# Kernel optimization log

Hardware: AMD Instinct MI355X
Metric: run time of the kernel (lower is better)

The kernel has to match this reference:

```python
import jax, jax.numpy as jnp
import numpy as np

B, C, H, W = 16, 256, 64, 64
K = 1024


def setup_inputs() -> dict:
    key = jax.random.key(0)
    k1, k2 = jax.random.split(key)
    z = jax.random.normal(k1, (B, C, H, W), dtype=jnp.float32)
    codebook = jax.random.normal(k2, (K, C), dtype=jnp.float32)
    return {"z": z, "codebook": codebook}


def reference(z, codebook):
    # assign: nearest-code indices via squared euclidean distance
    b, c, h, w = z.shape
    zf = jnp.transpose(z, (0, 2, 3, 1)).reshape(-1, c)            # [N, C]
    # ||z||^2 - 2 z.cb^T + ||cb||^2  -> [N, K]
    dists = (jnp.sum(zf * zf, axis=1, keepdims=True)
             - 2.0 * jnp.einsum('nc,kc->nk', zf, codebook)
             + jnp.sum(codebook * codebook, axis=1)[None, :])
    idx = jnp.argmin(dists, axis=1)                                # [N]
    indices = idx.reshape(b, 1, h, w)                              # [B,1,H,W]
    # embed_code: gather codebook rows, back to BCHW
    zq = codebook[idx].reshape(b, h, w, c)                         # [B,H,W,C]
    zq = jnp.transpose(zq, (0, 3, 1, 2))                           # [B,C,H,W]
    return zq, indices
```

## Files before the change

### kernel.cpp

```cpp
#include <hip/hip_runtime.h>


#define HWSZ 4096
#define CDIM 256
#define KCODES 1024
#define NPIX 65536
#define ZQ_ELEMS (16 * 256 * 4096)
#define MARGIN 0.75f

#define WS_CBSWZ 0
#define WS_CBN64 524288
#define WS_CBN32 532480
#define WS_CNT   536576
#define WS_LISTS 536592

typedef __attribute__((ext_vector_type(8))) short bf16x8;
typedef __attribute__((ext_vector_type(4))) float f32x4;
typedef __attribute__((ext_vector_type(4))) unsigned short us4;

#define MFMA16(a, b, c) __builtin_amdgcn_mfma_f32_16x16x32_bf16(a, b, c, 0, 0, 0)

__device__ __forceinline__ unsigned short f2bf(float f) {
  unsigned u = __float_as_uint(f);
  unsigned r = u + 0x7FFFu + ((u >> 16) & 1u);
  return (unsigned short)(r >> 16);
}

__device__ __forceinline__ void gload_lds16(const void* g, void* l) {
  __builtin_amdgcn_global_load_lds(
      (const __attribute__((address_space(1))) unsigned int*)g,
      (__attribute__((address_space(3))) unsigned int*)l, 16, 0, 0);
}

__device__ __forceinline__ void ins3(unsigned& k1, unsigned& k2, unsigned& k3,
                                     unsigned k) {
  unsigned nk2, nk3;
  asm("v_med3_u32 %0, %1, %2, %3" : "=v"(nk2) : "v"(k1), "v"(k2), "v"(k));
  asm("v_med3_u32 %0, %1, %2, %3" : "=v"(nk3) : "v"(k2), "v"(k3), "v"(k));
  k1 = k1 < k ? k1 : k;
  k2 = nk2;
  k3 = nk3;
}

__device__ __forceinline__ float keyf(unsigned k) {
  return __uint_as_float(k & 0xFFFFFC00u);
}

__global__ void vq_prep(const float* __restrict__ cb,
                        unsigned short* __restrict__ cbswz,
                        double* __restrict__ cbn64,
                        float* __restrict__ cbn32p,
                        int* __restrict__ cnt) {
  const int t = threadIdx.x;
  if (blockIdx.x == 0 && t == 0) { cnt[0] = 0; cnt[1] = 0; }
  const int code = blockIdx.x * 4 + (t >> 6);
  const int lane = t & 63;
  const int c4 = lane * 4;

  float4 v = *(const float4*)(cb + (size_t)code * CDIM + c4);
  us4 hv;
  hv.x = f2bf(-2.f * v.x); hv.y = f2bf(-2.f * v.y);
  hv.z = f2bf(-2.f * v.z); hv.w = f2bf(-2.f * v.w);
  const int K = (code >> 9) * 32 + ((code >> 4) & 31);
  const int kk = c4 >> 5;
  const int lg = (c4 >> 3) & 3;
  const int within = (c4 & 7) * 2;
  size_t off = (size_t)K * 8192 + kk * 1024 + (code & 15) * 64 + lg * 16 + within;
  *(us4*)((char*)cbswz + off) = hv;

  double s = (double)v.x * v.x;
  s = fma((double)v.y, (double)v.y, s);
  s = fma((double)v.z, (double)v.z, s);
  s = fma((double)v.w, (double)v.w, s);
#pragma unroll
  for (int o = 32; o; o >>= 1) s += __shfl_xor(s, o, 64);
  if (lane == 0) {
    cbn64[code] = s;
    cbn32p[code] = (float)s + 512.0f;
  }
}

__launch_bounds__(256)
__global__ void vq_stage1(const float* __restrict__ z,
                          const float* __restrict__ cb,
                          const unsigned short* __restrict__ cbswz,
                          const float* __restrict__ cbn32p,
                          float* __restrict__ out_zq,
                          float* __restrict__ out_idx,
                          int* __restrict__ cnt,
                          int* __restrict__ listA, int capA,
                          int* __restrict__ listB, int capB,
                          float* __restrict__ zws, int zcap) {
  extern __shared__ char smem[];
  const int t = threadIdx.x;
  const int w = t >> 6;
  const int lane = t & 63;
  const int lg = lane >> 4;
  const int lcode = lane & 15;
  const int h = w >> 1;
  const int q = w & 1;
  const int p0 = blockIdx.x * 64;
  const int b = p0 >> 12;
  const int hw0 = p0 & (HWSZ - 1);
  const float* zb = z + (size_t)b * (CDIM * HWSZ) + hw0;

  char* const bb0 = smem + q * 8192;
  char* const bb1 = smem + 16384 + q * 8192;
  char* const bb2 = smem + 32768 + q * 8192;
  float* nrm = (float*)(smem + 49152);
  char* scratch = smem + 49152;

  const int stl = h * 4096 + lane * 16;
  const char* cbbase = (const char*)cbswz + (size_t)q * 262144 + stl;

#define STAGE(CIDX, SBUF)                                             \
  {                                                                   \
    const char* gs_ = cbbase + ((size_t)(CIDX) << 13);                \
    char* ld_ = (SBUF) + stl;                                         \
    gload_lds16(gs_, ld_);                                            \
    gload_lds16(gs_ + 1024, ld_ + 1024);                              \
    gload_lds16(gs_ + 2048, ld_ + 2048);                              \
    gload_lds16(gs_ + 3072, ld_ + 3072);                              \
  }

  STAGE(0, bb0);
  STAGE(1, bb1);

  bf16x8 af[2][8];
#pragma unroll
  for (int T = 0; T < 2; ++T) {
    const float* zr = zb + (h * 32 + T * 16 + lcode);
#pragma unroll
    for (int kk = 0; kk < 8; ++kk) {
      const int ch0 = kk * 32 + lg * 8;
      bf16x8 f;
#pragma unroll
      for (int j = 0; j < 8; ++j)
        f[j] = (short)f2bf(zr[(size_t)(ch0 + j) * HWSZ]);
      af[T][kk] = f;
    }
  }

  *(float4*)(nrm + t * 4) = *(const float4*)(cbn32p + t * 4);
  __syncthreads();

  unsigned k1[2][4], k2[2][4], k3[2][4];
#pragma unroll
  for (int T = 0; T < 2; ++T)
#pragma unroll
    for (int q4 = 0; q4 < 4; ++q4) {
      k1[T][q4] = 0xFFFFFFFFu; k2[T][q4] = 0xFFFFFFFFu; k3[T][q4] = 0xFFFFFFFFu;
    }

  const int bq = lcode * 64 + lg * 16;
  const float* nrmp = nrm + q * 512 + lcode;
  const int kbase = q * 512 + lcode;

#define BODY(CIDX, RBUF, SBUF, DOSTAGE, WN)                           \
  {                                                                   \
    asm volatile("s_waitcnt vmcnt(" WN ")" ::: "memory");             \
    __builtin_amdgcn_s_barrier();                                     \
    __builtin_amdgcn_sched_barrier(0);                                \
    if (DOSTAGE) STAGE((CIDX) + 2, SBUF);                             \
    const char* pb_ = (RBUF) + bq;                                    \
    f32x4 acc0 = {0.f, 0.f, 0.f, 0.f};                                \
    f32x4 acc1 = {0.f, 0.f, 0.f, 0.f};                                \
    _Pragma("unroll")                                                 \
    for (int kk = 0; kk < 8; ++kk) {                                  \
      bf16x8 bf_ = *(const bf16x8*)(pb_ + kk * 1024);                 \
      acc0 = MFMA16(af[0][kk], bf_, acc0);                            \
      acc1 = MFMA16(af[1][kk], bf_, acc1);                            \
    }                                                                 \
    const unsigned code_ = (unsigned)(kbase + (CIDX) * 16);           \
    const float cn_ = nrmp[(CIDX) * 16];                              \
    _Pragma("unroll")                                                 \
    for (int q4 = 0; q4 < 4; ++q4) {                                  \
      float m0_ = cn_ + acc0[q4];                                     \
      ins3(k1[0][q4], k2[0][q4], k3[0][q4],                           \
           (__float_as_uint(m0_) & 0xFFFFFC00u) | code_);             \
      float m1_ = cn_ + acc1[q4];                                     \
      ins3(k1[1][q4], k2[1][q4], k3[1][q4],                           \
           (__float_as_uint(m1_) & 0xFFFFFC00u) | code_);             \
    }                                                                 \
  }

#pragma unroll 1
  for (int c3 = 0; c3 < 30; c3 += 3) {
    BODY(c3 + 0, bb0, bb2, 1, "4");
    BODY(c3 + 1, bb1, bb0, 1, "4");
    BODY(c3 + 2, bb2, bb1, 1, "4");
  }
  BODY(30, bb0, bb2, 0, "4");
  BODY(31, bb1, bb0, 0, "0");
#undef BODY
#undef STAGE

#pragma unroll
  for (int mask = 1; mask <= 8; mask <<= 1) {
#pragma unroll
    for (int T = 0; T < 2; ++T)
#pragma unroll
      for (int q4 = 0; q4 < 4; ++q4) {
        unsigned o1 = __shfl_xor(k1[T][q4], mask, 64);
        unsigned o2 = __shfl_xor(k2[T][q4], mask, 64);
        unsigned o3 = __shfl_xor(k3[T][q4], mask, 64);
        ins3(k1[T][q4], k2[T][q4], k3[T][q4], o1);
        ins3(k1[T][q4], k2[T][q4], k3[T][q4], o2);
        ins3(k1[T][q4], k2[T][q4], k3[T][q4], o3);
      }
  }

  unsigned* mk = (unsigned*)scratch;
  int* sbest = (int*)(scratch + 1536);
  int* flp = (int*)(scratch + 1792);
  int* flq = (int*)(scratch + 2048);
  int* lcnt = (int*)(scratch + 2304);
  if (t == 0) *lcnt = 0;
  if (lcode == 0) {
#pragma unroll
    for (int T = 0; T < 2; ++T)
#pragma unroll
      for (int q4 = 0; q4 < 4; ++q4) {
        int row = h * 32 + T * 16 + lg * 4 + q4;
        unsigned* d = mk + (row * 2 + q) * 3;
        d[0] = k1[T][q4]; d[1] = k2[T][q4]; d[2] = k3[T][q4];
      }
  }
  __syncthreads();

  if (t < 64) {
    unsigned a1 = mk[t * 6 + 0], a2 = mk[t * 6 + 1], a3 = mk[t * 6 + 2];
    ins3(a1, a2, a3, mk[t * 6 + 3]);
    ins3(a1, a2, a3, mk[t * 6 + 4]);
    ins3(a1, a2, a3, mk[t * 6 + 5]);
    const int p = p0 + t;
    const int i1 = (int)(a1 & 1023u);
    sbest[t] = i1;
    out_idx[p] = (float)i1;
    float f1 = keyf(a1);
    float g2 = keyf(a2) - f1;
    float g3 = keyf(a3) - f1;
    if (g3 < MARGIN) {
      int pos = atomicAdd(cnt + 1, 1);
      if (pos < capB) listB[pos] = p;
    } else if (g2 < MARGIN) {
      int pos = atomicAdd(cnt, 1);
      if (pos < capA) {
        listA[2 * pos] = p | (i1 << 16);
        listA[2 * pos + 1] = (int)(a2 & 1023u) | ((int)(a3 & 1023u) << 16);
        if (pos < zcap) {
          int li = atomicAdd(lcnt, 1);
          flp[li] = p;
          flq[li] = pos;
        }
      }
    }
  }
  __syncthreads();

  {
    const int px = t & 63;
    const int best = sbest[px];
    const int ch0g = (t >> 6) * 64;
    const float* crow = cb + (size_t)best * CDIM + ch0g;
    float* ob = out_zq + (size_t)b * (CDIM * HWSZ) + (size_t)ch0g * HWSZ + hw0 + px;
#pragma unroll 4
    for (int c2 = 0; c2 < 64; c2 += 4) {
      float4 v = *(const float4*)(crow + c2);
      ob[(size_t)(c2 + 0) * HWSZ] = v.x;
      ob[(size_t)(c2 + 1) * HWSZ] = v.y;
      ob[(size_t)(c2 + 2) * HWSZ] = v.z;
      ob[(size_t)(c2 + 3) * HWSZ] = v.w;
    }
  }

  {
    const int nf = *lcnt;
    for (int e = 0; e < nf; ++e) {
      const int p = flp[e];
      const int slot = flq[e];
      const int bb = p >> 12;
      const int hh = p & (HWSZ - 1);
      zws[(size_t)slot * 256 + t] =
          z[(size_t)bb * (CDIM * HWSZ) + (size_t)t * HWSZ + hh];
    }
  }
}

__launch_bounds__(256)
__global__ void vq_resolve3(const float* __restrict__ z,
                            const float* __restrict__ cb,
                            const double* __restrict__ cbn64,
                            float* __restrict__ out_zq,
                            float* __restrict__ out_idx,
                            const int* __restrict__ cnt,
                            const int* __restrict__ listA, int capA,
                            const float* __restrict__ zws, int zcap) {
  const int lane = threadIdx.x & 63;
  const int wid = (blockIdx.x * blockDim.x + threadIdx.x) >> 6;
  const int nw = (gridDim.x * blockDim.x) >> 6;
  int n = cnt[0];
  if (n > capA) n = capA;

  for (int i = wid; i < n; i += nw) {
    const int e0 = listA[2 * i];
    const int e1 = listA[2 * i + 1];
    const int p = e0 & 0xFFFF;
    int cand[3];
    cand[0] = (e0 >> 16) & 1023;
    cand[1] = e1 & 0xFFFF;
    cand[2] = (e1 >> 16) & 1023;
    const int b = p >> 12;
    const int hw = p & (HWSZ - 1);
    const int ch0 = lane * 4;

    double zv[4];
    if (i < zcap) {
      float4 zf = ((const float4*)(zws + (size_t)i * 256))[lane];
      zv[0] = (double)zf.x; zv[1] = (double)zf.y;
      zv[2] = (double)zf.z; zv[3] = (double)zf.w;
    } else {
      const float* zb = z + (size_t)b * (CDIM * HWSZ) + hw;
#pragma unroll
      for (int j = 0; j < 4; ++j) zv[j] = (double)zb[(size_t)(ch0 + j) * HWSZ];
    }

    double d[3];
#pragma unroll
    for (int tt = 0; tt < 3; ++tt) {
      float4 cv = *(const float4*)(cb + (size_t)cand[tt] * CDIM + ch0);
      double s = zv[0] * (double)cv.x;
      s = fma(zv[1], (double)cv.y, s);
      s = fma(zv[2], (double)cv.z, s);
      s = fma(zv[3], (double)cv.w, s);
#pragma unroll
      for (int off = 32; off; off >>= 1) s += __shfl_xor(s, off, 64);
      d[tt] = fma(-2.0, s, cbn64[cand[tt]]);
    }

    double bd = d[0];
    int bi = cand[0];
#pragma unroll
    for (int tt = 1; tt < 3; ++tt) {
      bool takes = (d[tt] < bd) || (d[tt] == bd && cand[tt] < bi);
      bd = takes ? d[tt] : bd;
      bi = takes ? cand[tt] : bi;
    }

    if (bi != cand[0]) {
      if (lane == 0) out_idx[p] = (float)bi;
      float4 cv = *(const float4*)(cb + (size_t)bi * CDIM + ch0);
      float* ob = out_zq + (size_t)b * (CDIM * HWSZ) + hw;
      ob[(size_t)(ch0 + 0) * HWSZ] = cv.x;
      ob[(size_t)(ch0 + 1) * HWSZ] = cv.y;
      ob[(size_t)(ch0 + 2) * HWSZ] = cv.z;
      ob[(size_t)(ch0 + 3) * HWSZ] = cv.w;
    }
  }
}

__launch_bounds__(256)
__global__ void vq_fullscan(const float* __restrict__ z,
                            const float* __restrict__ cb,
                            const double* __restrict__ cbn64,
                            float* __restrict__ out_zq,
                            float* __restrict__ out_idx,
                            const int* __restrict__ cnt,
                            const int* __restrict__ listB, int capB) {
  __shared__ double zl[256];
  __shared__ double sd[4];
  __shared__ int si[4];
  __shared__ int sfin;
  int n = cnt[1];
  if (n > capB) n = capB;
  const int t = threadIdx.x;
  const int w = t >> 6;
  const int lane = t & 63;

  for (int i = blockIdx.x; i < n; i += gridDim.x) {
    const int p = listB[i];
    const int b = p >> 12;
    const int hw = p & (HWSZ - 1);
    const float* zb = z + (size_t)b * (CDIM * HWSZ) + hw;
    zl[t] = (double)zb[(size_t)t * HWSZ];
    __syncthreads();

    const int g = t >> 2;
    const int sub = t & 3;
    const double* zq4 = zl + sub * 64;
    double bd = 1e300;
    int bi = 0;

    for (int j = 0; j < 16; ++j) {
      const int code = g + 64 * j;
      const float* crow = cb + (size_t)code * CDIM + sub * 64;
      double s = 0.0;
#pragma unroll
      for (int q4 = 0; q4 < 64; q4 += 4) {
        float4 cv = *(const float4*)(crow + q4);
        s = fma(zq4[q4 + 0], (double)cv.x, s);
        s = fma(zq4[q4 + 1], (double)cv.y, s);
        s = fma(zq4[q4 + 2], (double)cv.z, s);
        s = fma(zq4[q4 + 3], (double)cv.w, s);
      }
      s += __shfl_xor(s, 1, 64);
      s += __shfl_xor(s, 2, 64);
      double d = fma(-2.0, s, cbn64[code]);
      bool takes = (d < bd) || (d == bd && code < bi);
      bd = takes ? d : bd;
      bi = takes ? code : bi;
    }

#pragma unroll
    for (int off = 4; off <= 32; off <<= 1) {
      double od = __shfl_xor(bd, off, 64);
      int oi = __shfl_xor(bi, off, 64);
      bool takes = (od < bd) || (od == bd && oi < bi);
      bd = takes ? od : bd;
      bi = takes ? oi : bi;
    }
    if (lane == 0) { sd[w] = bd; si[w] = bi; }
    __syncthreads();
    if (t == 0) {
      double fd = sd[0];
      int fi = si[0];
#pragma unroll
      for (int k = 1; k < 4; ++k) {
        bool takes = (sd[k] < fd) || (sd[k] == fd && si[k] < fi);
        fd = takes ? sd[k] : fd;
        fi = takes ? si[k] : fi;
      }
      const int old = (int)out_idx[p];
      sfin = (fi != old) ? fi : -1;
      if (fi != old) out_idx[p] = (float)fi;
    }
    __syncthreads();
    const int best = sfin;
    if (best >= 0) {
      float* ob = out_zq + (size_t)b * (CDIM * HWSZ) + hw;
      ob[(size_t)t * HWSZ] = cb[(size_t)best * CDIM + t];
    }
    __syncthreads();
  }
}

extern "C" void kernel_launch(void* const* d_in, const int* in_sizes, int n_in,
                              void* d_out, int out_size, void* d_ws, size_t ws_size,
                              hipStream_t stream) {
  const float* z = (const float*)d_in[0];
  const float* cb = (const float*)d_in[1];
  float* out = (float*)d_out;
  float* out_zq = out;
  float* out_idx = out + ZQ_ELEMS;

  char* ws = (char*)d_ws;
  unsigned short* cbswz = (unsigned short*)(ws + WS_CBSWZ);
  double* cbn64 = (double*)(ws + WS_CBN64);
  float* cbn32p = (float*)(ws + WS_CBN32);
  int* cnt = (int*)(ws + WS_CNT);

  long long avail = (long long)ws_size - WS_LISTS;
  if (avail < 0) avail = 0;
  long long capA_ll = (avail / 4) / 8;
  if (capA_ll > NPIX) capA_ll = NPIX;
  int capA = (int)capA_ll;
  int* listA = (int*)(ws + WS_LISTS);
  long long rem = avail - (long long)capA * 8;
  long long capB_ll = rem / 8;
  if (capB_ll > NPIX) capB_ll = NPIX;
  if (capB_ll < 0) capB_ll = 0;
  int capB = (int)capB_ll;
  int* listB = (int*)(ws + WS_LISTS + (size_t)capA * 8);
  long long zoff = (WS_LISTS + (long long)capA * 8 + (long long)capB * 4 + 15) &
                   ~15LL;
  long long zcap_ll = ((long long)ws_size - zoff) / 1024;
  if (zcap_ll < 0) zcap_ll = 0;
  if (zcap_ll > capA) zcap_ll = capA;
  int zcap = (int)zcap_ll;
  float* zws = (float*)(ws + zoff);

  vq_prep<<<256, 256, 0, stream>>>(cb, cbswz, cbn64, cbn32p, cnt);
  vq_stage1<<<1024, 256, 53248, stream>>>(z, cb, cbswz, cbn32p, out_zq, out_idx,
                                          cnt, listA, capA, listB, capB,
                                          zws, zcap);
  vq_resolve3<<<1024, 256, 0, stream>>>(z, cb, cbn64, out_zq, out_idx,
                                        cnt, listA, capA, zws, zcap);
  vq_fullscan<<<256, 256, 0, stream>>>(z, cb, cbn64, out_zq, out_idx,
                                       cnt, listB, capB);
}
```

Measured before the change: 155.6 us.

## Double pixels per stage1 block to reuse codebook tiles across four MFMA rows

Each stage1 block now handles 128 pixels instead of 64, so every wave holds four 16-pixel A fragments and issues four MFMAs per codebook tile. Each LDS-staged codebook chunk is reused twice as much and the grid is halved. The change also seeds the accumulators with the code norm instead of adding it afterwards, prefetches the next norm, converts to bf16 with packed cvt instructions, and sets launch bounds for two blocks per CU. The cost is higher register pressure from 32 A fragments and 48 top-3 keys per thread, which may cause spills or lower occupancy, and fewer blocks in flight.

```diff
diff --git a/kernel.cpp b/kernel.cpp
--- a/kernel.cpp
+++ b/kernel.cpp
@@ -14,6 +14,15 @@
 #define WS_CNT   536576
 #define WS_LISTS 536592
 
+#define L_BUF0   0
+#define L_NRM    49152
+#define L_MK     53248
+#define L_SBEST  56320
+#define L_FLP    56832
+#define L_FLQ    57344
+#define L_LCNT   57856
+#define L_TOTAL  58368
+
 typedef __attribute__((ext_vector_type(8))) short bf16x8;
 typedef __attribute__((ext_vector_type(4))) float f32x4;
 typedef __attribute__((ext_vector_type(4))) unsigned short us4;
@@ -24,6 +33,12 @@
   unsigned u = __float_as_uint(f);
   unsigned r = u + 0x7FFFu + ((u >> 16) & 1u);
   return (unsigned short)(r >> 16);
+}
+
+__device__ __forceinline__ unsigned cvtpk(float lo, float hi) {
+  unsigned r;
+  asm("v_cvt_pk_bf16_f32 %0, %1, %2" : "=v"(r) : "v"(lo), "v"(hi));
+  return r;
 }
 
 __device__ __forceinline__ void gload_lds16(const void* g, void* l) {
@@ -80,7 +95,7 @@
   }
 }
 
-__launch_bounds__(256)
+__launch_bounds__(256, 2)
 __global__ void vq_stage1(const float* __restrict__ z,
                           const float* __restrict__ cb,
                           const unsigned short* __restrict__ cbswz,
@@ -99,7 +114,7 @@
   const int lcode = lane & 15;
   const int h = w >> 1;
   const int q = w & 1;
-  const int p0 = blockIdx.x * 64;
+  const int p0 = blockIdx.x * 128;
   const int b = p0 >> 12;
   const int hw0 = p0 & (HWSZ - 1);
   const float* zb = z + (size_t)b * (CDIM * HWSZ) + hw0;
@@ -107,8 +122,7 @@
   char* const bb0 = smem + q * 8192;
   char* const bb1 = smem + 16384 + q * 8192;
   char* const bb2 = smem + 32768 + q * 8192;
-  float* nrm = (float*)(smem + 49152);
-  char* scratch = smem + 49152;
+  float* nrm = (float*)(smem + L_NRM);
 
   const int stl = h * 4096 + lane * 16;
   const char* cbbase = (const char*)cbswz + (size_t)q * 262144 + stl;
@@ -126,17 +140,30 @@
   STAGE(0, bb0);
   STAGE(1, bb1);
 
-  bf16x8 af[2][8];
-#pragma unroll
-  for (int T = 0; T < 2; ++T) {
-    const float* zr = zb + (h * 32 + T * 16 + lcode);
+  bf16x8 af[4][8];
+#pragma unroll
+  for (int T = 0; T < 4; ++T) {
+    const float* zr = zb + (h * 64 + T * 16 + lcode);
 #pragma unroll
     for (int kk = 0; kk < 8; ++kk) {
       const int ch0 = kk * 32 + lg * 8;
+      float v0 = zr[(size_t)(ch0 + 0) * HWSZ];
+      float v1 = zr[(size_t)(ch0 + 1) * HWSZ];
+      float v2 = zr[(size_t)(ch0 + 2) * HWSZ];
+      float v3 = zr[(size_t)(ch0 + 3) * HWSZ];
+      float v4 = zr[(size_t)(ch0 + 4) * HWSZ];
+      float v5 = zr[(size_t)(ch0 + 5) * HWSZ];
+      float v6 = zr[(size_t)(ch0 + 6) * HWSZ];
+      float v7 = zr[(size_t)(ch0 + 7) * HWSZ];
+      unsigned p01 = cvtpk(v0, v1);
+      unsigned p23 = cvtpk(v2, v3);
+      unsigned p45 = cvtpk(v4, v5);
+      unsigned p67 = cvtpk(v6, v7);
       bf16x8 f;
-#pragma unroll
-      for (int j = 0; j < 8; ++j)
-        f[j] = (short)f2bf(zr[(size_t)(ch0 + j) * HWSZ]);
+      f[0] = (short)(p01 & 0xFFFF); f[1] = (short)(p01 >> 16);
+      f[2] = (short)(p23 & 0xFFFF); f[3] = (short)(p23 >> 16);
+      f[4] = (short)(p45 & 0xFFFF); f[5] = (short)(p45 >> 16);
+      f[6] = (short)(p67 & 0xFFFF); f[7] = (short)(p67 >> 16);
       af[T][kk] = f;
     }
   }
@@ -144,9 +171,9 @@
   *(float4*)(nrm + t * 4) = *(const float4*)(cbn32p + t * 4);
   __syncthreads();
 
-  unsigned k1[2][4], k2[2][4], k3[2][4];
-#pragma unroll
-  for (int T = 0; T < 2; ++T)
+  unsigned k1[4][4], k2[4][4], k3[4][4];
+#pragma unroll
+  for (int T = 0; T < 4; ++T)
 #pragma unroll
     for (int q4 = 0; q4 < 4; ++q4) {
       k1[T][q4] = 0xFFFFFFFFu; k2[T][q4] = 0xFFFFFFFFu; k3[T][q4] = 0xFFFFFFFFu;
@@ -155,32 +182,40 @@
   const int bq = lcode * 64 + lg * 16;
   const float* nrmp = nrm + q * 512 + lcode;
   const int kbase = q * 512 + lcode;
+  float cnn = nrmp[0];
 
 #define BODY(CIDX, RBUF, SBUF, DOSTAGE, WN)                           \
   {                                                                   \
     asm volatile("s_waitcnt vmcnt(" WN ")" ::: "memory");             \
     __builtin_amdgcn_s_barrier();                                     \
     __builtin_amdgcn_sched_barrier(0);                                \
+    const float cn_ = cnn;                                            \
+    if ((CIDX) < 31) cnn = nrmp[((CIDX) + 1) * 16];                   \
     if (DOSTAGE) STAGE((CIDX) + 2, SBUF);                             \
     const char* pb_ = (RBUF) + bq;                                    \
-    f32x4 acc0 = {0.f, 0.f, 0.f, 0.f};                                \
-    f32x4 acc1 = {0.f, 0.f, 0.f, 0.f};                                \
+    f32x4 a0 = {cn_, cn_, cn_, cn_};                                  \
+    f32x4 a1 = {cn_, cn_, cn_, cn_};                                  \
+    f32x4 a2 = {cn_, cn_, cn_, cn_};                                  \
+    f32x4 a3 = {cn_, cn_, cn_, cn_};                                  \
     _Pragma("unroll")                                                 \
     for (int kk = 0; kk < 8; ++kk) {                                  \
       bf16x8 bf_ = *(const bf16x8*)(pb_ + kk * 1024);                 \
-      acc0 = MFMA16(af[0][kk], bf_, acc0);                            \
-      acc1 = MFMA16(af[1][kk], bf_, acc1);                            \
+      a0 = MFMA16(af[0][kk], bf_, a0);                                \
+      a1 = MFMA16(af[1][kk], bf_, a1);                                \
+      a2 = MFMA16(af[2][kk], bf_, a2);                                \
+      a3 = MFMA16(af[3][kk], bf_, a3);                                \
     }                                                                 \
     const unsigned code_ = (unsigned)(kbase + (CIDX) * 16);           \
-    const float cn_ = nrmp[(CIDX) * 16];                              \
     _Pragma("unroll")                                                 \
     for (int q4 = 0; q4 < 4; ++q4) {                                  \
-      float m0_ = cn_ + acc0[q4];                                     \
       ins3(k1[0][q4], k2[0][q4], k3[0][q4],                           \
-           (__float_as_uint(m0_) & 0xFFFFFC00u) | code_);             \
-      float m1_ = cn_ + acc1[q4];                                     \
+           (__float_as_uint(a0[q4]) & 0xFFFFFC00u) | code_);          \
       ins3(k1[1][q4], k2[1][q4], k3[1][q4],                           \
-           (__float_as_uint(m1_) & 0xFFFFFC00u) | code_);             \
+           (__float_as_uint(a1[q4]) & 0xFFFFFC00u) | code_);          \
+      ins3(k1[2][q4], k2[2][q4], k3[2][q4],                           \
+           (__float_as_uint(a2[q4]) & 0xFFFFFC00u) | code_);          \
+      ins3(k1[3][q4], k2[3][q4], k3[3][q4],                           \
+           (__float_as_uint(a3[q4]) & 0xFFFFFC00u) | code_);          \
     }                                                                 \
   }
 
@@ -198,7 +233,7 @@
 #pragma unroll
   for (int mask = 1; mask <= 8; mask <<= 1) {
 #pragma unroll
-    for (int T = 0; T < 2; ++T)
+    for (int T = 0; T < 4; ++T)
 #pragma unroll
       for (int q4 = 0; q4 < 4; ++q4) {
         unsigned o1 = __shfl_xor(k1[T][q4], mask, 64);
@@ -210,25 +245,25 @@
       }
   }
 
-  unsigned* mk = (unsigned*)scratch;
-  int* sbest = (int*)(scratch + 1536);
-  int* flp = (int*)(scratch + 1792);
-  int* flq = (int*)(scratch + 2048);
-  int* lcnt = (int*)(scratch + 2304);
+  unsigned* mk = (unsigned*)(smem + L_MK);
+  int* sbest = (int*)(smem + L_SBEST);
+  int* flp = (int*)(smem + L_FLP);
+  int* flq = (int*)(smem + L_FLQ);
+  int* lcnt = (int*)(smem + L_LCNT);
   if (t == 0) *lcnt = 0;
   if (lcode == 0) {
 #pragma unroll
-    for (int T = 0; T < 2; ++T)
+    for (int T = 0; T < 4; ++T)
 #pragma unroll
       for (int q4 = 0; q4 < 4; ++q4) {
-        int row = h * 32 + T * 16 + lg * 4 + q4;
+        int row = h * 64 + T * 16 + lg * 4 + q4;
         unsigned* d = mk + (row * 2 + q) * 3;
         d[0] = k1[T][q4]; d[1] = k2[T][q4]; d[2] = k3[T][q4];
       }
   }
   __syncthreads();
 
-  if (t < 64) {
+  if (t < 128) {
     unsigned a1 = mk[t * 6 + 0], a2 = mk[t * 6 + 1], a3 = mk[t * 6 + 2];
     ins3(a1, a2, a3, mk[t * 6 + 3]);
     ins3(a1, a2, a3, mk[t * 6 + 4]);
@@ -259,13 +294,13 @@
   __syncthreads();
 
   {
-    const int px = t & 63;
+    const int px = t & 127;
     const int best = sbest[px];
-    const int ch0g = (t >> 6) * 64;
+    const int ch0g = (t >> 7) * 128;
     const float* crow = cb + (size_t)best * CDIM + ch0g;
     float* ob = out_zq + (size_t)b * (CDIM * HWSZ) + (size_t)ch0g * HWSZ + hw0 + px;
 #pragma unroll 4
-    for (int c2 = 0; c2 < 64; c2 += 4) {
+    for (int c2 = 0; c2 < 128; c2 += 4) {
       float4 v = *(const float4*)(crow + c2);
       ob[(size_t)(c2 + 0) * HWSZ] = v.x;
       ob[(size_t)(c2 + 1) * HWSZ] = v.y;
@@ -480,9 +515,9 @@
   float* zws = (float*)(ws + zoff);
 
   vq_prep<<<256, 256, 0, stream>>>(cb, cbswz, cbn64, cbn32p, cnt);
-  vq_stage1<<<1024, 256, 53248, stream>>>(z, cb, cbswz, cbn32p, out_zq, out_idx,
-                                          cnt, listA, capA, listB, capB,
-                                          zws, zcap);
+  vq_stage1<<<512, 256, L_TOTAL, stream>>>(z, cb, cbswz, cbn32p, out_zq, out_idx,
+                                           cnt, listA, capA, listB, capB,
+                                           zws, zcap);
   vq_resolve3<<<1024, 256, 0, stream>>>(z, cb, cbn64, out_zq, out_idx,
                                         cnt, listA, capA, zws, zcap);
   vq_fullscan<<<256, 256, 0, stream>>>(z, cb, cbn64, out_zq, out_idx,
```

Result: faster. 150.6 us (-3.2%).
